# Kernel tuning notes

Hardware: AMD Instinct MI355X
Metric: run time of the kernel (lower is better)

## Reference

```python
import jax, jax.numpy as jnp
import numpy as np

B, C, D = 1024, 1000, 256
EPS = 1e-4


def setup_inputs() -> dict:
    key = jax.random.key(0)
    k_z, k_mu = jax.random.split(key)
    z = jax.random.normal(k_z, (B, D), dtype=jnp.float32)
    mu = jax.random.normal(k_mu, (C, D), dtype=jnp.float32)  # init.normal_(mu, 0, 1)
    prior_logits = jnp.zeros((C,), dtype=jnp.float32)          # init.zeros_
    precision_factor = jnp.eye(D, dtype=jnp.float32)           # init.eye_
    return {"z": z, "mu": mu, "prior_logits": prior_logits,
            "precision_factor": precision_factor}


def reference(z, mu, prior_logits, precision_factor):
    # Shared precision matrix: symmetrized F F^T + eps I  -> (D, D)
    precision = precision_factor @ precision_factor.T
    precision = 0.5 * (precision + precision.T)
    precision = precision + EPS * jnp.eye(D, dtype=precision_factor.dtype)

    log_prior = jax.nn.log_softmax(prior_logits)  # (C,)

    # Mahalanobis distance per (sample, class): (z-mu)^T P (z-mu)
    diff = z[:, None, :] - mu[None, :, :]                      # (B, C, D)
    m2 = jnp.einsum('bcd,de,bce->bc', diff, precision, diff)   # (B, C)

    return log_prior[None, :] - 0.5 * m2
```

## Files before the change

### kernel.cpp

```cpp
#include <hip/hip_runtime.h>
#include <hip/hip_bf16.h>
#include <math.h>

constexpr int Bn = 1024;
constexpr int Cn = 1000;
constexpr int Dn = 256;
constexpr float EPS = 1e-4f;

typedef __attribute__((ext_vector_type(8))) short bf16x8;
typedef __attribute__((ext_vector_type(4))) float f32x4;

static __device__ __forceinline__ unsigned short f2bf(float x) {
    union { float f; unsigned u; } v; v.f = x;
    return (unsigned short)((v.u + 0x7fffu + ((v.u >> 16) & 1u)) >> 16);
}
static __device__ __forceinline__ float bf2f(unsigned short h) {
    union { unsigned u; float f; } v; v.u = ((unsigned)h) << 16; return v.f;
}
static __device__ __forceinline__ bf16x8 cvt8(const float4 lo, const float4 hi) {
    bf16x8 r;
    r[0] = (short)f2bf(lo.x); r[1] = (short)f2bf(lo.y);
    r[2] = (short)f2bf(lo.z); r[3] = (short)f2bf(lo.w);
    r[4] = (short)f2bf(hi.x); r[5] = (short)f2bf(hi.y);
    r[6] = (short)f2bf(hi.z); r[7] = (short)f2bf(hi.w);
    return r;
}

__global__ __launch_bounds__(256) void w_kernel2(const float* __restrict__ z,
                                                 const float* __restrict__ mu,
                                                 const float* __restrict__ logits,
                                                 const float* __restrict__ F,
                                                 unsigned short* __restrict__ Wb,
                                                 float* __restrict__ rn_part,
                                                 float* __restrict__ epsn,
                                                 float* __restrict__ lse_p) {
    const int bid = blockIdx.x, tid = threadIdx.x;

    if (bid == 512) {
        if (tid < 64) {
            float mx = -INFINITY;
            for (int i = tid; i < Cn; i += 64) mx = fmaxf(mx, logits[i]);
#pragma unroll
            for (int off = 32; off > 0; off >>= 1) mx = fmaxf(mx, __shfl_xor(mx, off));
            float sm = 0.f;
            for (int i = tid; i < Cn; i += 64) sm += expf(logits[i] - mx);
#pragma unroll
            for (int off = 32; off > 0; off >>= 1) sm += __shfl_xor(sm, off);
            if (tid == 0) *lse_p = mx + logf(sm);
        }
        return;
    }

    const int row0 = (bid >> 3) * 32;
    const int col0 = (bid & 7) * 32;
    const int lane = tid & 63, w = tid >> 6;
    const int la = lane & 15, kg = lane >> 4;
    const int wr = (w >> 1) * 16, wc = (w & 1) * 16;
    const int ct = (bid & 7) * 2 + (w & 1);

    const int grow = row0 + wr + la;
    const float* ap = (grow < 1024) ? &z[(size_t)grow * Dn]
                                    : &mu[(size_t)min(grow - 1024, Cn - 1) * Dn];
    bf16x8 af[8];
    float zs = 0.f;
#pragma unroll
    for (int kt = 0; kt < 8; ++kt) {
        const int k0 = kt * 32 + kg * 8;
        af[kt] = cvt8(*(const float4*)&ap[k0], *(const float4*)&ap[k0 + 4]);
#pragma unroll
        for (int j = 0; j < 8; ++j) {
            const float v = bf2f((unsigned short)af[kt][j]);
            zs = fmaf(v, v, zs);
        }
    }

    const int bcol = col0 + wc + la;
    f32x4 acc = {0.f, 0.f, 0.f, 0.f};
#pragma unroll
    for (int kt = 0; kt < 8; ++kt) {
        const int k0 = kt * 32 + kg * 8;
        bf16x8 bf;
#pragma unroll
        for (int j = 0; j < 8; ++j) bf[j] = (short)f2bf(F[(size_t)(k0 + j) * Dn + bcol]);
        acc = __builtin_amdgcn_mfma_f32_16x16x32_bf16(af[kt], bf, acc, 0, 0, 0);
    }

    float np[4];
#pragma unroll
    for (int j = 0; j < 4; ++j) {
        const unsigned short h = f2bf(acc[j]);
        Wb[(size_t)(row0 + wr + kg * 4 + j) * Dn + bcol] = h;
        const float v = bf2f(h);
        float s = v * v;
        s += __shfl_xor(s, 1); s += __shfl_xor(s, 2);
        s += __shfl_xor(s, 4); s += __shfl_xor(s, 8);
        np[j] = s;
    }
    if (la == 0) {
#pragma unroll
        for (int j = 0; j < 4; ++j)
            rn_part[(size_t)(row0 + wr + kg * 4 + j) * 16 + ct] = np[j];
    }

    zs += __shfl_xor(zs, 16);
    zs += __shfl_xor(zs, 32);
    if ((bid & 7) == 0 && (w & 1) == 0 && kg == 0)
        epsn[row0 + wr + la] = EPS * zs;
}

__global__ __launch_bounds__(256) void out_kernel(const unsigned short* __restrict__ Wb,
                                                  const float* __restrict__ rn_part,
                                                  const float* __restrict__ epsn,
                                                  const float* __restrict__ logits,
                                                  const float* __restrict__ lse_p,
                                                  float* __restrict__ out) {
    __shared__ float rowbias[32], colbias[64];
    const int bid = blockIdx.x, tid = threadIdx.x;
    const int row0 = (bid >> 4) * 32;
    const int col0 = (bid & 15) * 64;

    if (tid < 32) {
        const int r = row0 + tid;
        const float4* p = (const float4*)&rn_part[(size_t)r * 16];
        const float4 a = p[0], b = p[1], c = p[2], d = p[3];
        const float s = a.x + a.y + a.z + a.w + b.x + b.y + b.z + b.w +
                        c.x + c.y + c.z + c.w + d.x + d.y + d.z + d.w;
        rowbias[tid] = -0.5f * (s + epsn[r]);
    } else if (tid < 96) {
        const int lc = tid - 32, c = col0 + lc;
        float v = 0.f;
        if (c < Cn) {
            const int r = 1024 + c;
            const float4* p = (const float4*)&rn_part[(size_t)r * 16];
            const float4 a = p[0], b = p[1], cc = p[2], d = p[3];
            const float s = a.x + a.y + a.z + a.w + b.x + b.y + b.z + b.w +
                            cc.x + cc.y + cc.z + cc.w + d.x + d.y + d.z + d.w;
            v = logits[c] - *lse_p - 0.5f * (s + epsn[r]);
        }
        colbias[lc] = v;
    }
    __syncthreads();

    const int lane = tid & 63, w = tid >> 6;
    const int la = lane & 15, kg = lane >> 4;
    const int wr = (w >> 1) * 16, wc = (w & 1) * 32;

    const bf16x8* pa  = (const bf16x8*)&Wb[(size_t)(row0 + wr + la) * Dn + kg * 8];
    const bf16x8* pb0 = (const bf16x8*)&Wb[(size_t)(1024 + col0 + wc + la) * Dn + kg * 8];
    const bf16x8* pb1 = pb0 + 512;

    f32x4 c0 = {0.f, 0.f, 0.f, 0.f}, c1 = {0.f, 0.f, 0.f, 0.f};
#pragma unroll
    for (int kt = 0; kt < 8; ++kt) {
        const bf16x8 a  = pa[kt * 4];
        const bf16x8 b0 = pb0[kt * 4];
        const bf16x8 b1 = pb1[kt * 4];
        c0 = __builtin_amdgcn_mfma_f32_16x16x32_bf16(a, b0, c0, 0, 0, 0);
        c1 = __builtin_amdgcn_mfma_f32_16x16x32_bf16(a, b1, c1, 0, 0, 0);
    }

#pragma unroll
    for (int j = 0; j < 4; ++j) {
        const int rl = wr + kg * 4 + j;
        const int gr = row0 + rl;
        const float rb = rowbias[rl];
        const int gc0 = col0 + wc + la;
        const int gc1 = gc0 + 16;
        if (gc0 < Cn) out[(size_t)gr * Cn + gc0] = c0[j] + rb + colbias[wc + la];
        if (gc1 < Cn) out[(size_t)gr * Cn + gc1] = c1[j] + rb + colbias[wc + 16 + la];
    }
}

extern "C" void kernel_launch(void* const* d_in, const int* in_sizes, int n_in,
                              void* d_out, int out_size, void* d_ws, size_t ws_size,
                              hipStream_t stream) {
    const float* z      = (const float*)d_in[0];
    const float* mu     = (const float*)d_in[1];
    const float* logits = (const float*)d_in[2];
    const float* F      = (const float*)d_in[3];
    float* out = (float*)d_out;

    char* ws = (char*)d_ws;
    unsigned short* Wb = (unsigned short*)(ws);
    float* rn_part = (float*)(ws + (1 << 20));
    float* epsn    = (float*)(ws + (1 << 20) + (128 << 10));
    float* lse     = epsn + 2048;

    w_kernel2<<<dim3(513), dim3(256), 0, stream>>>(z, mu, logits, F, Wb, rn_part, epsn, lse);
    out_kernel<<<dim3(512), dim3(256), 0, stream>>>(Wb, rn_part, epsn, logits, lse, out);
}
```

Before: 22.63 us.

## Fuse projection and output GEMM into one kernel with flag-based inter-block sync

Merges the two-kernel pipeline into a single launch of 512 blocks. Each block first computes a 16-row by 64-column slice of the bf16 projected matrix and its partial row norms, then publishes a release flag. It then waits on the flags for the row and column tiles it needs before running the output MFMA GEMM. The log-sum-exp of the logits is recomputed in every block instead of in a dedicated extra block. This removes a kernel launch boundary and lets the second phase start per tile rather than after a global barrier. The spin-wait needs all blocks to be co-resident. Because the flags are never reset between calls, later invocations may not actually wait for the current call's producers.

```diff
diff --git a/kernel.cpp b/kernel.cpp
--- a/kernel.cpp
+++ b/kernel.cpp
@@ -6,6 +6,7 @@
 constexpr int Cn = 1000;
 constexpr int Dn = 256;
 constexpr float EPS = 1e-4f;
+constexpr unsigned SENTINEL = 0x5A17C0DEu;
 
 typedef __attribute__((ext_vector_type(8))) short bf16x8;
 typedef __attribute__((ext_vector_type(4))) float f32x4;
@@ -26,127 +27,124 @@
     return r;
 }
 
-__global__ __launch_bounds__(256) void w_kernel2(const float* __restrict__ z,
-                                                 const float* __restrict__ mu,
-                                                 const float* __restrict__ logits,
-                                                 const float* __restrict__ F,
-                                                 unsigned short* __restrict__ Wb,
-                                                 float* __restrict__ rn_part,
-                                                 float* __restrict__ epsn,
-                                                 float* __restrict__ lse_p) {
+__global__ __launch_bounds__(256, 2) void lda_pipe(const float* __restrict__ z,
+                                                   const float* __restrict__ mu,
+                                                   const float* __restrict__ logits,
+                                                   const float* __restrict__ F,
+                                                   unsigned short* __restrict__ Wb,
+                                                   float* __restrict__ rn_part,
+                                                   float* __restrict__ epsn,
+                                                   unsigned* __restrict__ flags,
+                                                   float* __restrict__ out) {
+    __shared__ float rowbias[32], colbias[64];
     const int bid = blockIdx.x, tid = threadIdx.x;
-
-    if (bid == 512) {
-        if (tid < 64) {
-            float mx = -INFINITY;
-            for (int i = tid; i < Cn; i += 64) mx = fmaxf(mx, logits[i]);
-#pragma unroll
-            for (int off = 32; off > 0; off >>= 1) mx = fmaxf(mx, __shfl_xor(mx, off));
-            float sm = 0.f;
-            for (int i = tid; i < Cn; i += 64) sm += expf(logits[i] - mx);
-#pragma unroll
-            for (int off = 32; off > 0; off >>= 1) sm += __shfl_xor(sm, off);
-            if (tid == 0) *lse_p = mx + logf(sm);
-        }
-        return;
-    }
-
-    const int row0 = (bid >> 3) * 32;
-    const int col0 = (bid & 7) * 32;
     const int lane = tid & 63, w = tid >> 6;
     const int la = lane & 15, kg = lane >> 4;
-    const int wr = (w >> 1) * 16, wc = (w & 1) * 16;
-    const int ct = (bid & 7) * 2 + (w & 1);
 
-    const int grow = row0 + wr + la;
-    const float* ap = (grow < 1024) ? &z[(size_t)grow * Dn]
-                                    : &mu[(size_t)min(grow - 1024, Cn - 1) * Dn];
-    bf16x8 af[8];
-    float zs = 0.f;
+    {
+        const int rg = bid >> 2, cq = bid & 3;
+        const int grow = rg * 16 + la;
+        const float* ap = (grow < 1024) ? &z[(size_t)grow * Dn]
+                                        : &mu[(size_t)min(grow - 1024, Cn - 1) * Dn];
+        bf16x8 af[8];
+        float zs = 0.f;
 #pragma unroll
-    for (int kt = 0; kt < 8; ++kt) {
-        const int k0 = kt * 32 + kg * 8;
-        af[kt] = cvt8(*(const float4*)&ap[k0], *(const float4*)&ap[k0 + 4]);
+        for (int kt = 0; kt < 8; ++kt) {
+            const int k0 = kt * 32 + kg * 8;
+            af[kt] = cvt8(*(const float4*)&ap[k0], *(const float4*)&ap[k0 + 4]);
 #pragma unroll
-        for (int j = 0; j < 8; ++j) {
-            const float v = bf2f((unsigned short)af[kt][j]);
-            zs = fmaf(v, v, zs);
+            for (int j = 0; j < 8; ++j) {
+                const float v = bf2f((unsigned short)af[kt][j]);
+                zs = fmaf(v, v, zs);
+            }
+        }
+        const int bcol = cq * 64 + w * 16 + la;
+        f32x4 acc = {0.f, 0.f, 0.f, 0.f};
+#pragma unroll
+        for (int kt = 0; kt < 8; ++kt) {
+            const int k0 = kt * 32 + kg * 8;
+            bf16x8 bf;
+#pragma unroll
+            for (int j = 0; j < 8; ++j) bf[j] = (short)f2bf(F[(size_t)(k0 + j) * Dn + bcol]);
+            acc = __builtin_amdgcn_mfma_f32_16x16x32_bf16(af[kt], bf, acc, 0, 0, 0);
+        }
+        float np[4];
+#pragma unroll
+        for (int j = 0; j < 4; ++j) {
+            const unsigned short h = f2bf(acc[j]);
+            Wb[(size_t)(rg * 16 + kg * 4 + j) * Dn + bcol] = h;
+            const float v = bf2f(h);
+            float s = v * v;
+            s += __shfl_xor(s, 1); s += __shfl_xor(s, 2);
+            s += __shfl_xor(s, 4); s += __shfl_xor(s, 8);
+            np[j] = s;
+        }
+        if (la == 0) {
+#pragma unroll
+            for (int j = 0; j < 4; ++j)
+                rn_part[(size_t)(rg * 16 + kg * 4 + j) * 16 + cq * 4 + w] = np[j];
+        }
+        zs += __shfl_xor(zs, 16);
+        zs += __shfl_xor(zs, 32);
+        if (cq == 0 && w == 0 && kg == 0) epsn[rg * 16 + la] = EPS * zs;
+
+        __syncthreads();
+        if (tid == 0) {
+            __threadfence();
+            __hip_atomic_store(&flags[bid], SENTINEL, __ATOMIC_RELEASE,
+                               __HIP_MEMORY_SCOPE_AGENT);
         }
     }
 
-    const int bcol = col0 + wc + la;
-    f32x4 acc = {0.f, 0.f, 0.f, 0.f};
+    const int r = bid >> 4;
+    const int c = bid & 15;
+
+    float lse = 0.f;
+    if (w < 2) {
+        float mx = -INFINITY;
+        for (int i = lane; i < Cn; i += 64) mx = fmaxf(mx, logits[i]);
 #pragma unroll
-    for (int kt = 0; kt < 8; ++kt) {
-        const int k0 = kt * 32 + kg * 8;
-        bf16x8 bf;
+        for (int off = 32; off > 0; off >>= 1) mx = fmaxf(mx, __shfl_xor(mx, off));
+        float sm = 0.f;
+        for (int i = lane; i < Cn; i += 64) sm += expf(logits[i] - mx);
 #pragma unroll
-        for (int j = 0; j < 8; ++j) bf[j] = (short)f2bf(F[(size_t)(k0 + j) * Dn + bcol]);
-        acc = __builtin_amdgcn_mfma_f32_16x16x32_bf16(af[kt], bf, acc, 0, 0, 0);
+        for (int off = 32; off > 0; off >>= 1) sm += __shfl_xor(sm, off);
+        lse = mx + logf(sm);
     }
 
-    float np[4];
-#pragma unroll
-    for (int j = 0; j < 4; ++j) {
-        const unsigned short h = f2bf(acc[j]);
-        Wb[(size_t)(row0 + wr + kg * 4 + j) * Dn + bcol] = h;
-        const float v = bf2f(h);
-        float s = v * v;
-        s += __shfl_xor(s, 1); s += __shfl_xor(s, 2);
-        s += __shfl_xor(s, 4); s += __shfl_xor(s, 8);
-        np[j] = s;
+    if (tid < 24) {
+        const int fi = (tid < 8) ? (8 * r + tid)
+                                 : (256 + 16 * c + (tid - 8));
+        while (__hip_atomic_load(&flags[fi], __ATOMIC_ACQUIRE,
+                                 __HIP_MEMORY_SCOPE_AGENT) != SENTINEL) {}
     }
-    if (la == 0) {
-#pragma unroll
-        for (int j = 0; j < 4; ++j)
-            rn_part[(size_t)(row0 + wr + kg * 4 + j) * 16 + ct] = np[j];
-    }
-
-    zs += __shfl_xor(zs, 16);
-    zs += __shfl_xor(zs, 32);
-    if ((bid & 7) == 0 && (w & 1) == 0 && kg == 0)
-        epsn[row0 + wr + la] = EPS * zs;
-}
-
-__global__ __launch_bounds__(256) void out_kernel(const unsigned short* __restrict__ Wb,
-                                                  const float* __restrict__ rn_part,
-                                                  const float* __restrict__ epsn,
-                                                  const float* __restrict__ logits,
-                                                  const float* __restrict__ lse_p,
-                                                  float* __restrict__ out) {
-    __shared__ float rowbias[32], colbias[64];
-    const int bid = blockIdx.x, tid = threadIdx.x;
-    const int row0 = (bid >> 4) * 32;
-    const int col0 = (bid & 15) * 64;
+    __syncthreads();
 
     if (tid < 32) {
-        const int r = row0 + tid;
-        const float4* p = (const float4*)&rn_part[(size_t)r * 16];
-        const float4 a = p[0], b = p[1], c = p[2], d = p[3];
+        const int rr = r * 32 + tid;
+        const float4* p = (const float4*)&rn_part[(size_t)rr * 16];
+        const float4 a = p[0], b = p[1], cc = p[2], d = p[3];
         const float s = a.x + a.y + a.z + a.w + b.x + b.y + b.z + b.w +
-                        c.x + c.y + c.z + c.w + d.x + d.y + d.z + d.w;
-        rowbias[tid] = -0.5f * (s + epsn[r]);
+                        cc.x + cc.y + cc.z + cc.w + d.x + d.y + d.z + d.w;
+        rowbias[tid] = -0.5f * (s + epsn[rr]);
     } else if (tid < 96) {
-        const int lc = tid - 32, c = col0 + lc;
+        const int lc = tid - 32, gc = c * 64 + lc;
         float v = 0.f;
-        if (c < Cn) {
-            const int r = 1024 + c;
-            const float4* p = (const float4*)&rn_part[(size_t)r * 16];
+        if (gc < Cn) {
+            const int rr = 1024 + gc;
+            const float4* p = (const float4*)&rn_part[(size_t)rr * 16];
             const float4 a = p[0], b = p[1], cc = p[2], d = p[3];
             const float s = a.x + a.y + a.z + a.w + b.x + b.y + b.z + b.w +
                             cc.x + cc.y + cc.z + cc.w + d.x + d.y + d.z + d.w;
-            v = logits[c] - *lse_p - 0.5f * (s + epsn[r]);
+            v = logits[gc] - lse - 0.5f * (s + epsn[rr]);
         }
         colbias[lc] = v;
     }
     __syncthreads();
 
-    const int lane = tid & 63, w = tid >> 6;
-    const int la = lane & 15, kg = lane >> 4;
     const int wr = (w >> 1) * 16, wc = (w & 1) * 32;
-
-    const bf16x8* pa  = (const bf16x8*)&Wb[(size_t)(row0 + wr + la) * Dn + kg * 8];
-    const bf16x8* pb0 = (const bf16x8*)&Wb[(size_t)(1024 + col0 + wc + la) * Dn + kg * 8];
+    const bf16x8* pa  = (const bf16x8*)&Wb[(size_t)(r * 32 + wr + la) * Dn + kg * 8];
+    const bf16x8* pb0 = (const bf16x8*)&Wb[(size_t)(1024 + c * 64 + wc + la) * Dn + kg * 8];
     const bf16x8* pb1 = pb0 + 512;
 
     f32x4 c0 = {0.f, 0.f, 0.f, 0.f}, c1 = {0.f, 0.f, 0.f, 0.f};
@@ -162,9 +160,9 @@
 #pragma unroll
     for (int j = 0; j < 4; ++j) {
         const int rl = wr + kg * 4 + j;
-        const int gr = row0 + rl;
+        const int gr = r * 32 + rl;
         const float rb = rowbias[rl];
-        const int gc0 = col0 + wc + la;
+        const int gc0 = c * 64 + wc + la;
         const int gc1 = gc0 + 16;
         if (gc0 < Cn) out[(size_t)gr * Cn + gc0] = c0[j] + rb + colbias[wc + la];
         if (gc1 < Cn) out[(size_t)gr * Cn + gc1] = c1[j] + rb + colbias[wc + 16 + la];
@@ -184,8 +182,8 @@
     unsigned short* Wb = (unsigned short*)(ws);
     float* rn_part = (float*)(ws + (1 << 20));
     float* epsn    = (float*)(ws + (1 << 20) + (128 << 10));
-    float* lse     = epsn + 2048;
+    unsigned* flags = (unsigned*)(ws + (1 << 20) + (136 << 10));
 
-    w_kernel2<<<dim3(513), dim3(256), 0, stream>>>(z, mu, logits, F, Wb, rn_part, epsn, lse);
-    out_kernel<<<dim3(512), dim3(256), 0, stream>>>(Wb, rn_part, epsn, logits, lse, out);
+    lda_pipe<<<dim3(512), dim3(256), 0, stream>>>(z, mu, logits, F,
+                                                  Wb, rn_part, epsn, flags, out);
 }
```

Result: slower. 46.14 us (+103.9%).
